# Kernel tuning notes

Measured on AMD Instinct MI355X. Metric: run time of the kernel, lower is better.

The kernel has to match this reference:

```python
import jax, jax.numpy as jnp
import numpy as np

N = 4096
IN_F = 256
F = 64      # out_features
H = 4       # heads
NEG_SLOPE = 0.2


def setup_inputs() -> dict:
    key = jax.random.key(0)
    k1, k2, k3, k4 = jax.random.split(key, 4)
    x = jax.random.normal(k1, (N, IN_F), dtype=jnp.float32)
    # symmetric random binary adjacency with self-loops (avoids empty softmax rows)
    adj = jax.random.bernoulli(k2, 0.5, (N, N)).astype(jnp.float32)
    adj = jnp.clip(adj + adj.T, 0.0, 1.0)
    adj = jnp.maximum(adj, jnp.eye(N, dtype=jnp.float32))
    W = jax.random.normal(k3, (IN_F, F * H), dtype=jnp.float32) * (1.0 / np.sqrt(IN_F))
    a = jax.random.normal(k4, (2 * F, 1), dtype=jnp.float32) * 0.1
    return {"x": x, "adj": adj, "W": W, "a": a}


def reference(x, adj, W, a):
    # h: [N, H, F]
    h = (x @ W).reshape(N, H, F)
    # e[i, j, h] = leakyrelu(a_l . h[i, h] + a_r . h[j, h])  -- avoids the O(N^2*H*2F) concat
    a_l = a[:F, 0]
    a_r = a[F:, 0]
    el = jnp.einsum('nhf,f->nh', h, a_l)  # [N, H]
    er = jnp.einsum('nhf,f->nh', h, a_r)  # [N, H]
    e = jax.nn.leaky_relu(el[:, None, :] + er[None, :, :], NEG_SLOPE)  # [N, N, H]
    e = jnp.where(adj[:, :, None] == 0, -jnp.inf, e)
    attention = jax.nn.softmax(e, axis=1)  # softmax over neighbors j
    h_prime = jnp.einsum('ijh,jhf->ihf', attention, h)  # [N, H, F]
    return h_prime.mean(axis=1)  # [N, F]  (heads > 1 -> mean over heads)
```

## Files before the change

### kernel.cpp

```cpp
#include <hip/hip_runtime.h>
#include <hip/hip_bf16.h>

#define NN 4096
#define LOG2E 1.44269504088896340736f

typedef __attribute__((ext_vector_type(8))) short s8v;
typedef __attribute__((ext_vector_type(4))) float f4v;

__device__ __forceinline__ unsigned fu(float x){ union{float f;unsigned u;}z; z.f=x; return z.u; }
__device__ __forceinline__ unsigned short f2bf_rne(float x){
  unsigned u = fu(x);
  u += 0x7fffu + ((u >> 16) & 1u);
  return (unsigned short)(u >> 16);
}
__device__ __forceinline__ unsigned pack2_rne(float a, float b){
  return (unsigned)f2bf_rne(a) | ((unsigned)f2bf_rne(b) << 16);
}

__global__ __launch_bounds__(256) void k1_proj(
    const float* __restrict__ x, const float* __restrict__ W,
    const float* __restrict__ a, unsigned short* __restrict__ Vf,
    float* __restrict__ el4, float* __restrict__ Qr, float* __restrict__ Sr)
{
  __shared__ float4 xs[512];
  const int t = threadIdx.x;
  const int r0 = blockIdx.x * 8;
  const float4* xg = (const float4*)(x + (size_t)r0 * 256);
  xs[t] = xg[t];
  xs[t + 256] = xg[t + 256];
  __syncthreads();

  float acc[8] = {0.f,0.f,0.f,0.f,0.f,0.f,0.f,0.f};
  const float* Wp = W + t;
  float wa0 = Wp[0],    wa1 = Wp[256],  wa2 = Wp[512],  wa3 = Wp[768];
  float wb0 = Wp[1024], wb1 = Wp[1280], wb2 = Wp[1536], wb3 = Wp[1792];
  #pragma unroll 1
  for (int k4 = 0; k4 < 64; ++k4) {
    const int kn = (k4 + 2) & 63;
    float nw0 = Wp[kn*1024 +   0];
    float nw1 = Wp[kn*1024 + 256];
    float nw2 = Wp[kn*1024 + 512];
    float nw3 = Wp[kn*1024 + 768];
    #pragma unroll
    for (int r = 0; r < 8; ++r) {
      float4 xv = xs[r*64 + k4];
      acc[r] = fmaf(xv.x, wa0, acc[r]);
      acc[r] = fmaf(xv.y, wa1, acc[r]);
      acc[r] = fmaf(xv.z, wa2, acc[r]);
      acc[r] = fmaf(xv.w, wa3, acc[r]);
    }
    wa0 = wb0; wa1 = wb1; wa2 = wb2; wa3 = wb3;
    wb0 = nw0; wb1 = nw1; wb2 = nw2; wb3 = nw3;
  }

  union { unsigned u[4]; s8v v; } pk;
  #pragma unroll
  for (int p = 0; p < 4; ++p)
    pk.u[p] = pack2_rne(acc[2*p], acc[2*p+1]);
  {
    const int hh = t >> 6, nf = (t >> 4) & 3, mm = t & 15;
    const int jblk = r0 >> 5, qq = (r0 >> 3) & 3;
    const size_t chunk = (size_t)(((hh * 128 + jblk) * 4 + nf) * 64 + qq * 16 + mm);
    *(s8v*)(Vf + chunk * 8) = pk.v;
  }

  const int f = t & 63, h = t >> 6;
  const float al = a[f], ar = a[64 + f];
  #pragma unroll
  for (int r = 0; r < 8; ++r) {
    float v = acc[r] * al;
    float u = acc[r] * ar;
    #pragma unroll
    for (int off = 32; off > 0; off >>= 1) {
      v += __shfl_xor(v, off);
      u += __shfl_xor(u, off);
    }
    if (f == 0) {
      el4[(r0 + r) * 4 + h] = v * LOG2E;
      float up = u * LOG2E;
      Qr[h * NN + (r0 + r)] = __builtin_amdgcn_exp2f(up);
      Sr[h * NN + (r0 + r)] = __builtin_amdgcn_exp2f(0.2f * up);
    }
  }
}

__global__ __launch_bounds__(256, 4) void k0_pack(
    const float* __restrict__ adj, const float* __restrict__ el4,
    const float* __restrict__ Qr, const float* __restrict__ Sr,
    unsigned long long* __restrict__ adjB, float* __restrict__ lsumP)
{
  __shared__ float qsh[8192];
  const int t = threadIdx.x;
  const int w = t >> 6, l = t & 63;
  const int row = blockIdx.x * 4 + w;
  const int p4 = blockIdx.y;
  const int jbase = p4 * 1024;

  const float* arow = adj + (size_t)row * NN + jbase + l * 4;
  float4 av0 = *(const float4*)(arow);
  float4 av1 = *(const float4*)(arow + 256);
  float4 av2 = *(const float4*)(arow + 512);
  float4 av3 = *(const float4*)(arow + 768);

  {
    const int h = t >> 6;
    #pragma unroll
    for (int k = 0; k < 4; ++k) {
      float4 qv = *(const float4*)(Qr + h * NN + jbase + k * 256 + l * 4);
      float4 sv = *(const float4*)(Sr + h * NN + jbase + k * 256 + l * 4);
      *(float4*)(qsh + ((k * 2 + 0) * 4 + h) * 256 + l * 4) = qv;
      *(float4*)(qsh + ((k * 2 + 1) * 4 + h) * 256 + l * 4) = sv;
    }
  }

  {
    unsigned long long* dst = adjB + (size_t)row * 64 + p4 * 16;
    const float4 avs[4] = {av0, av1, av2, av3};
    #pragma unroll
    for (int k = 0; k < 4; ++k) {
      unsigned long long b0 = __ballot(avs[k].x != 0.0f);
      unsigned long long b1 = __ballot(avs[k].y != 0.0f);
      unsigned long long b2 = __ballot(avs[k].z != 0.0f);
      unsigned long long b3 = __ballot(avs[k].w != 0.0f);
      if (l == 0) {
        dst[k * 4 + 0] = b0; dst[k * 4 + 1] = b1;
        dst[k * 4 + 2] = b2; dst[k * 4 + 3] = b3;
      }
    }
  }

  float4 elv = *(const float4*)(el4 + row * 4);
  const float P[4] = { __builtin_amdgcn_exp2f(elv.x), __builtin_amdgcn_exp2f(elv.y),
                       __builtin_amdgcn_exp2f(elv.z), __builtin_amdgcn_exp2f(elv.w) };
  const float R[4] = { __builtin_amdgcn_exp2f(0.2f*elv.x), __builtin_amdgcn_exp2f(0.2f*elv.y),
                       __builtin_amdgcn_exp2f(0.2f*elv.z), __builtin_amdgcn_exp2f(0.2f*elv.w) };

  __syncthreads();

  float ls[4] = {0.f, 0.f, 0.f, 0.f};
  {
    const float4 avs[4] = {av0, av1, av2, av3};
    #pragma unroll
    for (int k = 0; k < 4; ++k) {
      const float4 av = avs[k];
      #pragma unroll
      for (int h = 0; h < 4; ++h) {
        float4 qv = *(const float4*)(qsh + ((k * 2 + 0) * 4 + h) * 256 + l * 4);
        float4 sv = *(const float4*)(qsh + ((k * 2 + 1) * 4 + h) * 256 + l * 4);
        float s;
        s = av.x * fmaxf(P[h] * qv.x, R[h] * sv.x);
        s = fmaf(av.y, fmaxf(P[h] * qv.y, R[h] * sv.y), s);
        s = fmaf(av.z, fmaxf(P[h] * qv.z, R[h] * sv.z), s);
        s = fmaf(av.w, fmaxf(P[h] * qv.w, R[h] * sv.w), s);
        ls[h] += s;
      }
    }
  }
  #pragma unroll
  for (int h = 0; h < 4; ++h) {
    float v = ls[h];
    #pragma unroll
    for (int off = 32; off > 0; off >>= 1) v += __shfl_xor(v, off);
    ls[h] = v;
  }
  if (l == 0)
    *(float4*)(lsumP + ((size_t)p4 * NN + row) * 4) = make_float4(ls[0], ls[1], ls[2], ls[3]);
}

__global__ __launch_bounds__(256, 2) void k2_attn(
    const unsigned long long* __restrict__ adjB, const unsigned short* __restrict__ Vf,
    const float* __restrict__ el4, const float* __restrict__ lsumP,
    const float* __restrict__ Qr, const float* __restrict__ Sr,
    float* __restrict__ out)
{
  __shared__ float qs[8192];
  const int t = threadIdx.x;
  const int w = t >> 6, l = t & 63;
  const int m = l & 15, q = l >> 4;
  const int i0 = blockIdx.x * 32;
  const int sw = blockIdx.y * 4 + w;
  const int jwin = sw * 256;

  {
    const int jc = l >> 3, qq = (l >> 1) & 3, hp = (l & 1) * 4;
    #pragma unroll
    for (int h = 0; h < 4; ++h) {
      float4 qv = *(const float4*)(Qr + h * NN + jwin + l * 4);
      float4 sv = *(const float4*)(Sr + h * NN + jwin + l * 4);
      float* cell = qs + (((w * 4 + h) * 8 + jc) * 4 + qq) * 16;
      *(float4*)(cell + hp) = qv;
      *(float4*)(cell + 8 + hp) = sv;
    }
  }

  float Pl[2][4], Rl[2][4];
  unsigned long long bm[2][4];
  #pragma unroll
  for (int s = 0; s < 2; ++s) {
    const int i = i0 + s * 16 + m;
    float4 elv = *(const float4*)(el4 + i * 4);
    float lx = 0.f, ly = 0.f, lz = 0.f, lw = 0.f;
    #pragma unroll
    for (int p = 0; p < 4; ++p) {
      float4 v = *(const float4*)(lsumP + ((size_t)p * NN + i) * 4);
      lx += v.x; ly += v.y; lz += v.z; lw += v.w;
    }
    const float el_[4] = {elv.x, elv.y, elv.z, elv.w};
    const float lv_[4] = {lx, ly, lz, lw};
    #pragma unroll
    for (int h = 0; h < 4; ++h) {
      const float inv = 1.0f / lv_[h];
      Pl[s][h] = __builtin_amdgcn_exp2f(el_[h]) * inv;
      Rl[s][h] = __builtin_amdgcn_exp2f(0.2f * el_[h]) * inv;
    }
    const unsigned long long* bp = adjB + (size_t)i * 64 + sw * 4;
    bm[s][0] = bp[0]; bm[s][1] = bp[1]; bm[s][2] = bp[2]; bm[s][3] = bp[3];
  }

  f4v acc[2][4];
  #pragma unroll
  for (int s = 0; s < 2; ++s)
    #pragma unroll
    for (int nf = 0; nf < 4; ++nf) acc[s][nf] = (f4v){0.f, 0.f, 0.f, 0.f};

  const s8v* vfp = (const s8v*)Vf;
  s8v Bc[4];
  #pragma unroll
  for (int nf = 0; nf < 4; ++nf)
    Bc[nf] = vfp[(size_t)((0 * 128 + sw * 8 + 0) * 4 + nf) * 64 + l];

  #pragma unroll 1
  for (int jc = 0; jc < 8; ++jc) {
    const unsigned sh = jc * 8 + q * 2;
    float bitf[2][8];
    #pragma unroll
    for (int s = 0; s < 2; ++s) {
      const unsigned t0 = (unsigned)(bm[s][0] >> sh) & 3u;
      const unsigned t1 = (unsigned)(bm[s][1] >> sh) & 3u;
      const unsigned t2 = (unsigned)(bm[s][2] >> sh) & 3u;
      const unsigned t3 = (unsigned)(bm[s][3] >> sh) & 3u;
      bitf[s][0] = (float)(t0 & 1u); bitf[s][4] = (float)(t0 >> 1);
      bitf[s][1] = (float)(t1 & 1u); bitf[s][5] = (float)(t1 >> 1);
      bitf[s][2] = (float)(t2 & 1u); bitf[s][6] = (float)(t2 >> 1);
      bitf[s][3] = (float)(t3 & 1u); bitf[s][7] = (float)(t3 >> 1);
    }

    #pragma unroll
    for (int h = 0; h < 4; ++h) {
      const int hn = (h < 3) ? h + 1 : 0;
      const int jcn = (h < 3) ? jc : jc + 1;
      s8v Bn[4];
      #pragma unroll
      for (int nf = 0; nf < 4; ++nf)
        Bn[nf] = vfp[(size_t)((hn * 128 + sw * 8 + jcn) * 4 + nf) * 64 + l];

      const float* cell = qs + (((w * 4 + h) * 8 + jc) * 4 + q) * 16;
      float4 q0  = *(const float4*)(cell);
      float4 q1  = *(const float4*)(cell + 4);
      float4 sv0 = *(const float4*)(cell + 8);
      float4 sv1 = *(const float4*)(cell + 12);
      #pragma unroll
      for (int s = 0; s < 2; ++s) {
        const float Ph = Pl[s][h], Rh = Rl[s][h];
        float s0 = bitf[s][0] * fmaxf(Ph * q0.x, Rh * sv0.x);
        float s1 = bitf[s][1] * fmaxf(Ph * q0.y, Rh * sv0.y);
        float s2 = bitf[s][2] * fmaxf(Ph * q0.z, Rh * sv0.z);
        float s3 = bitf[s][3] * fmaxf(Ph * q0.w, Rh * sv0.w);
        float s4 = bitf[s][4] * fmaxf(Ph * q1.x, Rh * sv1.x);
        float s5 = bitf[s][5] * fmaxf(Ph * q1.y, Rh * sv1.y);
        float s6 = bitf[s][6] * fmaxf(Ph * q1.z, Rh * sv1.z);
        float s7 = bitf[s][7] * fmaxf(Ph * q1.w, Rh * sv1.w);
        union { unsigned u[4]; s8v v; } A;
        A.u[0] = pack2_rne(s0, s1);
        A.u[1] = pack2_rne(s2, s3);
        A.u[2] = pack2_rne(s4, s5);
        A.u[3] = pack2_rne(s6, s7);
        #pragma unroll
        for (int nf = 0; nf < 4; ++nf)
          acc[s][nf] = __builtin_amdgcn_mfma_f32_16x16x32_bf16(A.v, Bc[nf], acc[s][nf], 0, 0, 0);
      }
      #pragma unroll
      for (int nf = 0; nf < 4; ++nf) Bc[nf] = Bn[nf];
    }
  }

  __syncthreads();
  if (w > 0) {
    float* dst = qs + ((w - 1) * 64 + l) * 36;
    #pragma unroll
    for (int s = 0; s < 2; ++s)
      #pragma unroll
      for (int nf = 0; nf < 4; ++nf)
        *(f4v*)(dst + (s * 4 + nf) * 4) = acc[s][nf];
  }
  __syncthreads();
  if (w == 0) {
    #pragma unroll
    for (int s = 0; s < 2; ++s)
      #pragma unroll
      for (int nf = 0; nf < 4; ++nf) {
        f4v sum = acc[s][nf];
        #pragma unroll
        for (int ww = 0; ww < 3; ++ww)
          sum += *(const f4v*)(qs + (ww * 64 + l) * 36 + (s * 4 + nf) * 4);
        #pragma unroll
        for (int r = 0; r < 4; ++r) {
          int row = i0 + s * 16 + q * 4 + r;
          int col = nf * 16 + m;
          atomicAdd(&out[row * 64 + col], 0.25f * sum[r]);
        }
      }
  }
}

extern "C" void kernel_launch(void* const* d_in, const int* in_sizes, int n_in,
                              void* d_out, int out_size, void* d_ws, size_t ws_size,
                              hipStream_t stream) {
  const float* x   = (const float*)d_in[0];
  const float* adj = (const float*)d_in[1];
  const float* W   = (const float*)d_in[2];
  const float* a   = (const float*)d_in[3];
  float* out = (float*)d_out;

  char* ws = (char*)d_ws;
  unsigned short* Vf = (unsigned short*)ws;
  float* el4   = (float*)(ws + (2u << 20));
  float* Qr    = (float*)(ws + (2u << 20) + (64u << 10));
  float* Sr    = (float*)(ws + (2u << 20) + (128u << 10));
  float* lsumP = (float*)(ws + (2u << 20) + (192u << 10));
  unsigned long long* adjB = (unsigned long long*)(ws + (2u << 20) + (448u << 10));

  hipMemsetAsync(out, 0, (size_t)out_size * sizeof(float), stream);
  k1_proj<<<512, 256, 0, stream>>>(x, W, a, Vf, el4, Qr, Sr);
  k0_pack<<<dim3(1024, 4), 256, 0, stream>>>(adj, el4, Qr, Sr, adjB, lsumP);
  k2_attn<<<dim3(128, 4), 256, 0, stream>>>(adjB, Vf, el4, lsumP, Qr, Sr, out);
}
```

Before: 155.2 us.

## Restructure attention kernel to share j-window across waves with LDS-staged V double buffering

Each block now covers 128 rows with one 256-column j window shared by all four waves, instead of 32 rows split over four j windows. V fragments are loaded through asynchronous global-to-LDS copies into a double buffer, and waves read B operands from LDS. The LDS cross-wave reduction is removed, so each wave issues its own atomics. The software RNE bf16 pack is replaced by the hardware v_cvt_pk_bf16_f32 instruction. Costs are more LDS use, more global atomics and barriers inside the loop.

Result: no change. 157.0 us (+1.1%).

```diff
diff --git a/kernel.cpp b/kernel.cpp
--- a/kernel.cpp
+++ b/kernel.cpp
@@ -15,6 +15,15 @@
 }
 __device__ __forceinline__ unsigned pack2_rne(float a, float b){
   return (unsigned)f2bf_rne(a) | ((unsigned)f2bf_rne(b) << 16);
+}
+__device__ __forceinline__ unsigned cvtpk(float a, float b){
+  unsigned r;
+  asm("v_cvt_pk_bf16_f32 %0, %1, %2" : "=v"(r) : "v"(a), "v"(b));
+  return r;
+}
+__device__ __forceinline__ void gload_lds16(const void* g, void* lds){
+  __builtin_amdgcn_global_load_lds((const __attribute__((address_space(1))) unsigned*)g,
+                                   (__attribute__((address_space(3))) unsigned*)lds, 16, 0, 0);
 }
 
 __global__ __launch_bounds__(256) void k1_proj(
@@ -173,12 +182,12 @@
     const float* __restrict__ Qr, const float* __restrict__ Sr,
     float* __restrict__ out)
 {
-  __shared__ float qs[8192];
+  __shared__ float smem[2048 + 2 * 8192];
   const int t = threadIdx.x;
   const int w = t >> 6, l = t & 63;
   const int m = l & 15, q = l >> 4;
-  const int i0 = blockIdx.x * 32;
-  const int sw = blockIdx.y * 4 + w;
+  const int i0 = blockIdx.x * 128 + w * 32;
+  const int sw = blockIdx.y;
   const int jwin = sw * 256;
 
   {
@@ -187,7 +196,7 @@
     for (int h = 0; h < 4; ++h) {
       float4 qv = *(const float4*)(Qr + h * NN + jwin + l * 4);
       float4 sv = *(const float4*)(Sr + h * NN + jwin + l * 4);
-      float* cell = qs + (((w * 4 + h) * 8 + jc) * 4 + qq) * 16;
+      float* cell = smem + ((h * 8 + jc) * 4 + qq) * 16;
       *(float4*)(cell + hp) = qv;
       *(float4*)(cell + 8 + hp) = sv;
     }
@@ -223,94 +232,93 @@
     #pragma unroll
     for (int nf = 0; nf < 4; ++nf) acc[s][nf] = (f4v){0.f, 0.f, 0.f, 0.f};
 
-  const s8v* vfp = (const s8v*)Vf;
-  s8v Bc[4];
-  #pragma unroll
-  for (int nf = 0; nf < 4; ++nf)
-    Bc[nf] = vfp[(size_t)((0 * 128 + sw * 8 + 0) * 4 + nf) * 64 + l];
+#define STAGE(gi, pb) { \
+    const size_t c0 = ((size_t)(w * 512 + sw * 32 + 8 * (gi))) * 64 + l; \
+    float* ldsb = smem + 2048 + (pb) * 8192 + w * 2048 + l * 4; \
+    _Pragma("unroll") \
+    for (int k = 0; k < 8; ++k) \
+      gload_lds16(Vf + (c0 + k * 64) * 8, ldsb + k * 256); \
+  }
+
+  STAGE(0, 0);
+  STAGE(1, 1);
 
   #pragma unroll 1
-  for (int jc = 0; jc < 8; ++jc) {
-    const unsigned sh = jc * 8 + q * 2;
-    float bitf[2][8];
-    #pragma unroll
-    for (int s = 0; s < 2; ++s) {
-      const unsigned t0 = (unsigned)(bm[s][0] >> sh) & 3u;
-      const unsigned t1 = (unsigned)(bm[s][1] >> sh) & 3u;
-      const unsigned t2 = (unsigned)(bm[s][2] >> sh) & 3u;
-      const unsigned t3 = (unsigned)(bm[s][3] >> sh) & 3u;
-      bitf[s][0] = (float)(t0 & 1u); bitf[s][4] = (float)(t0 >> 1);
-      bitf[s][1] = (float)(t1 & 1u); bitf[s][5] = (float)(t1 >> 1);
-      bitf[s][2] = (float)(t2 & 1u); bitf[s][6] = (float)(t2 >> 1);
-      bitf[s][3] = (float)(t3 & 1u); bitf[s][7] = (float)(t3 >> 1);
-    }
-
-    #pragma unroll
-    for (int h = 0; h < 4; ++h) {
-      const int hn = (h < 3) ? h + 1 : 0;
-      const int jcn = (h < 3) ? jc : jc + 1;
-      s8v Bn[4];
-      #pragma unroll
-      for (int nf = 0; nf < 4; ++nf)
-        Bn[nf] = vfp[(size_t)((hn * 128 + sw * 8 + jcn) * 4 + nf) * 64 + l];
-
-      const float* cell = qs + (((w * 4 + h) * 8 + jc) * 4 + q) * 16;
-      float4 q0  = *(const float4*)(cell);
-      float4 q1  = *(const float4*)(cell + 4);
-      float4 sv0 = *(const float4*)(cell + 8);
-      float4 sv1 = *(const float4*)(cell + 12);
+  for (int g = 0; g < 4; ++g) {
+    const int pb = g & 1;
+    if (g < 3) asm volatile("s_waitcnt vmcnt(8)" ::: "memory");
+    else       asm volatile("s_waitcnt vmcnt(0)" ::: "memory");
+    __syncthreads();
+
+    #pragma unroll
+    for (int jc2 = 0; jc2 < 2; ++jc2) {
+      const int jc = 2 * g + jc2;
+      const unsigned sh = jc * 8 + q * 2;
+      float bitf[2][8];
       #pragma unroll
       for (int s = 0; s < 2; ++s) {
-        const float Ph = Pl[s][h], Rh = Rl[s][h];
-        float s0 = bitf[s][0] * fmaxf(Ph * q0.x, Rh * sv0.x);
-        float s1 = bitf[s][1] * fmaxf(Ph * q0.y, Rh * sv0.y);
-        float s2 = bitf[s][2] * fmaxf(Ph * q0.z, Rh * sv0.z);
-        float s3 = bitf[s][3] * fmaxf(Ph * q0.w, Rh * sv0.w);
-        float s4 = bitf[s][4] * fmaxf(Ph * q1.x, Rh * sv1.x);
-        float s5 = bitf[s][5] * fmaxf(Ph * q1.y, Rh * sv1.y);
-        float s6 = bitf[s][6] * fmaxf(Ph * q1.z, Rh * sv1.z);
-        float s7 = bitf[s][7] * fmaxf(Ph * q1.w, Rh * sv1.w);
-        union { unsigned u[4]; s8v v; } A;
-        A.u[0] = pack2_rne(s0, s1);
-        A.u[1] = pack2_rne(s2, s3);
-        A.u[2] = pack2_rne(s4, s5);
-        A.u[3] = pack2_rne(s6, s7);
+        const unsigned t0 = (unsigned)(bm[s][0] >> sh) & 3u;
+        const unsigned t1 = (unsigned)(bm[s][1] >> sh) & 3u;
+        const unsigned t2 = (unsigned)(bm[s][2] >> sh) & 3u;
+        const unsigned t3 = (unsigned)(bm[s][3] >> sh) & 3u;
+        bitf[s][0] = (float)(t0 & 1u); bitf[s][4] = (float)(t0 >> 1);
+        bitf[s][1] = (float)(t1 & 1u); bitf[s][5] = (float)(t1 >> 1);
+        bitf[s][2] = (float)(t2 & 1u); bitf[s][6] = (float)(t2 >> 1);
+        bitf[s][3] = (float)(t3 & 1u); bitf[s][7] = (float)(t3 >> 1);
+      }
+
+      #pragma unroll
+      for (int h = 0; h < 4; ++h) {
+        const float* bfrag = smem + 2048 + pb * 8192 + ((h * 2 + jc2) * 4) * 256 + l * 4;
+        s8v B0 = *(const s8v*)(bfrag);
+        s8v B1 = *(const s8v*)(bfrag + 256);
+        s8v B2 = *(const s8v*)(bfrag + 512);
+        s8v B3 = *(const s8v*)(bfrag + 768);
+
+        const float* cell = smem + ((h * 8 + jc) * 4 + q) * 16;
+        float4 q0  = *(const float4*)(cell);
+        float4 q1  = *(const float4*)(cell + 4);
+        float4 sv0 = *(const float4*)(cell + 8);
+        float4 sv1 = *(const float4*)(cell + 12);
         #pragma unroll
-        for (int nf = 0; nf < 4; ++nf)
-          acc[s][nf] = __builtin_amdgcn_mfma_f32_16x16x32_bf16(A.v, Bc[nf], acc[s][nf], 0, 0, 0);
-      }
+        for (int s = 0; s < 2; ++s) {
+          const float Ph = Pl[s][h], Rh = Rl[s][h];
+          float s0 = bitf[s][0] * fmaxf(Ph * q0.x, Rh * sv0.x);
+          float s1 = bitf[s][1] * fmaxf(Ph * q0.y, Rh * sv0.y);
+          float s2 = bitf[s][2] * fmaxf(Ph * q0.z, Rh * sv0.z);
+          float s3 = bitf[s][3] * fmaxf(Ph * q0.w, Rh * sv0.w);
+          float s4 = bitf[s][4] * fmaxf(Ph * q1.x, Rh * sv1.x);
+          float s5 = bitf[s][5] * fmaxf(Ph * q1.y, Rh * sv1.y);
+          float s6 = bitf[s][6] * fmaxf(Ph * q1.z, Rh * sv1.z);
+          float s7 = bitf[s][7] * fmaxf(Ph * q1.w, Rh * sv1.w);
+          union { unsigned u[4]; s8v v; } A;
+          A.u[0] = cvtpk(s0, s1);
+          A.u[1] = cvtpk(s2, s3);
+          A.u[2] = cvtpk(s4, s5);
+          A.u[3] = cvtpk(s6, s7);
+          acc[s][0] = __builtin_amdgcn_mfma_f32_16x16x32_bf16(A.v, B0, acc[s][0], 0, 0, 0);
+          acc[s][1] = __builtin_amdgcn_mfma_f32_16x16x32_bf16(A.v, B1, acc[s][1], 0, 0, 0);
+          acc[s][2] = __builtin_amdgcn_mfma_f32_16x16x32_bf16(A.v, B2, acc[s][2], 0, 0, 0);
+          acc[s][3] = __builtin_amdgcn_mfma_f32_16x16x32_bf16(A.v, B3, acc[s][3], 0, 0, 0);
+        }
+      }
+    }
+
+    __syncthreads();
+    if (g < 2) STAGE(g + 2, pb);
+  }
+#undef STAGE
+
+  #pragma unroll
+  for (int s = 0; s < 2; ++s)
+    #pragma unroll
+    for (int nf = 0; nf < 4; ++nf)
       #pragma unroll
-      for (int nf = 0; nf < 4; ++nf) Bc[nf] = Bn[nf];
-    }
-  }
-
-  __syncthreads();
-  if (w > 0) {
-    float* dst = qs + ((w - 1) * 64 + l) * 36;
-    #pragma unroll
-    for (int s = 0; s < 2; ++s)
-      #pragma unroll
-      for (int nf = 0; nf < 4; ++nf)
-        *(f4v*)(dst + (s * 4 + nf) * 4) = acc[s][nf];
-  }
-  __syncthreads();
-  if (w == 0) {
-    #pragma unroll
-    for (int s = 0; s < 2; ++s)
-      #pragma unroll
-      for (int nf = 0; nf < 4; ++nf) {
-        f4v sum = acc[s][nf];
-        #pragma unroll
-        for (int ww = 0; ww < 3; ++ww)
-          sum += *(const f4v*)(qs + (ww * 64 + l) * 36 + (s * 4 + nf) * 4);
-        #pragma unroll
-        for (int r = 0; r < 4; ++r) {
-          int row = i0 + s * 16 + q * 4 + r;
-          int col = nf * 16 + m;
-          atomicAdd(&out[row * 64 + col], 0.25f * sum[r]);
-        }
-      }
-  }
+      for (int r = 0; r < 4; ++r) {
+        int row = i0 + s * 16 + q * 4 + r;
+        int col = nf * 16 + m;
+        atomicAdd(&out[row * 64 + col], 0.25f * acc[s][nf][r]);
+      }
 }
 
 extern "C" void kernel_launch(void* const* d_in, const int* in_sizes, int n_in,
@@ -333,5 +341,5 @@
   hipMemsetAsync(out, 0, (size_t)out_size * sizeof(float), stream);
   k1_proj<<<512, 256, 0, stream>>>(x, W, a, Vf, el4, Qr, Sr);
   k0_pack<<<dim3(1024, 4), 256, 0, stream>>>(adj, el4, Qr, Sr, adjB, lsumP);
-  k2_attn<<<dim3(128, 4), 256, 0, stream>>>(adjB, Vf, el4, lsumP, Qr, Sr, out);
-}
+  k2_attn<<<dim3(32, 16), 256, 0, stream>>>(adjB, Vf, el4, lsumP, Qr, Sr, out);
+}
```
